# Kernel optimization log

Measured on AMD Instinct MI355X. Metric: run time of the kernel, lower is better.

Reference implementation:

```python
import jax, jax.numpy as jnp
import numpy as np

B, T, C, H = 4, 2048, 1024, 16
D = C // H  # head_dim = 64
ROPE_BASE = 10000.0


def _rope_cos_sin(T, D, dtype):
    # inv_freq: (D/2,), freqs: (T, D/2) -> cos/sin tiled to (T, D)
    inv_freq = 1.0 / (ROPE_BASE ** (jnp.arange(0, D, 2, dtype=jnp.float32) / D))
    freqs = jnp.arange(T, dtype=jnp.float32)[:, None] * inv_freq[None, :]
    emb = jnp.concatenate([freqs, freqs], axis=-1)  # (T, D)
    return jnp.cos(emb).astype(dtype), jnp.sin(emb).astype(dtype)


def _rotate_half(x):
    x1, x2 = jnp.split(x, 2, axis=-1)
    return jnp.concatenate([-x2, x1], axis=-1)


def setup_inputs() -> dict:
    key = jax.random.key(0)
    k1, k2, k3 = jax.random.split(key, 3)
    x = jax.random.normal(k1, (B, T, C), dtype=jnp.float32)
    W_qkv = jax.random.normal(k2, (C, 3 * C), dtype=jnp.float32) * (C ** -0.5)
    b_qkv = jnp.zeros((3 * C,), dtype=jnp.float32)
    W_out = jax.random.normal(k3, (C, C), dtype=jnp.float32) * (C ** -0.5)
    b_out = jnp.zeros((C,), dtype=jnp.float32)
    return {"x": x, "W_qkv": W_qkv, "b_qkv": b_qkv, "W_out": W_out, "b_out": b_out}


def reference(x, W_qkv, b_qkv, W_out, b_out):
    Bx, Tx, Cx = x.shape
    qkv = x @ W_qkv + b_qkv                                   # (B, T, 3C)
    qkv = qkv.reshape(Bx, Tx, 3, H, D).transpose(2, 0, 3, 1, 4)  # (3, B, H, T, D)
    q, k, v = qkv[0], qkv[1], qkv[2]

    cos, sin = _rope_cos_sin(Tx, D, x.dtype)                  # (T, D) each
    q = q * cos + _rotate_half(q) * sin
    k = k * cos + _rotate_half(k) * sin

    # NOTE: original code has no 1/sqrt(D) scaling — faithful reproduction.
    att = jnp.einsum('bhtd,bhsd->bhts', q, k)                 # (B, H, T, T)
    causal = jnp.tril(jnp.ones((Tx, Tx), dtype=bool))
    att = jnp.where(causal[None, None, :, :], att, -jnp.inf)
    att = jax.nn.softmax(att, axis=-1)
    y = jnp.einsum('bhts,bhsd->bhtd', att, v)                 # (B, H, T, D)
    y = y.transpose(0, 2, 1, 3).reshape(Bx, Tx, Cx)
    return y @ W_out + b_out
```

## Files before the change

kernel.cpp:

```cpp
#include <hip/hip_runtime.h>
#include <math.h>

#define NB    4
#define T_SEQ 2048
#define CDIM  1024
#define NH    16
#define DH    64
#define NQKV  3072

typedef short bf16x8 __attribute__((ext_vector_type(8)));
typedef float f32x4  __attribute__((ext_vector_type(4)));

#define GLOBAL_AS __attribute__((address_space(1)))
#define LDS_AS    __attribute__((address_space(3)))

__device__ __forceinline__ void async16(const void* g, void* l) {
  __builtin_amdgcn_global_load_lds((const GLOBAL_AS void*)g, (LDS_AS void*)l, 16, 0, 0);
}

__device__ __forceinline__ unsigned short f2bf(float f) {
  unsigned u = __float_as_uint(f);
  unsigned r = u + 0x7FFF + ((u >> 16) & 1);
  return (unsigned short)(r >> 16);
}

#define SWZ8(row, c) ((((row) << 3) | ((c) ^ ((row) & 7))) << 3)

#define BARRIER()  asm volatile("s_barrier" ::: "memory")
#define VMCNT(n)   asm volatile("s_waitcnt vmcnt(" #n ")" ::: "memory")

__device__ __forceinline__ void transpose_tile32(
    const float* __restrict__ in, unsigned short* __restrict__ out,
    int K, int N, int bx, int by, float (*tile)[33], int tid) {
  int n0 = bx << 5, k0 = by << 5;
  int r  = tid >> 3;
  int c4 = (tid & 7) << 2;
  float4 v = *(const float4*)&in[(size_t)(k0 + r) * N + n0 + c4];
  tile[r][c4 + 0] = v.x; tile[r][c4 + 1] = v.y;
  tile[r][c4 + 2] = v.z; tile[r][c4 + 3] = v.w;
  __syncthreads();
  ushort4 o;
  o.x = f2bf(tile[c4 + 0][r]); o.y = f2bf(tile[c4 + 1][r]);
  o.z = f2bf(tile[c4 + 2][r]); o.w = f2bf(tile[c4 + 3][r]);
  *(ushort4*)&out[(size_t)(n0 + r) * K + k0 + c4] = o;
}

__global__ __launch_bounds__(256) void prep_fused(
    const float* __restrict__ x, unsigned short* __restrict__ xb,
    const float* __restrict__ W_qkv, unsigned short* __restrict__ wqt,
    const float* __restrict__ W_out, unsigned short* __restrict__ wot,
    float2* __restrict__ rope) {
  __shared__ float tile[32][33];
  int blk = blockIdx.x;
  int tid = threadIdx.x;
  if (blk < 8192) {
    int i = blk * 256 + tid;
    float4 v = ((const float4*)x)[i];
    ushort4 o;
    o.x = f2bf(v.x); o.y = f2bf(v.y); o.z = f2bf(v.z); o.w = f2bf(v.w);
    ((ushort4*)xb)[i] = o;
  } else if (blk < 11264) {
    int local = blk - 8192;
    transpose_tile32(W_qkv, wqt, CDIM, NQKV, local % 96, local / 96, tile, tid);
  } else if (blk < 12288) {
    int local = blk - 11264;
    transpose_tile32(W_out, wot, CDIM, CDIM, local & 31, local >> 5, tile, tid);
  } else {
    int i = (blk - 12288) * 256 + tid;
    int t = i >> 5, d = i & 31;
    float inv = expf((float)d * -0.28782313662425572f);
    float s, c;
    sincosf((float)t * inv, &s, &c);
    rope[i] = make_float2(c, s);
  }
}

#define STAGE(kt, b)                                                          \
  { const unsigned short* sa_ = aSrc + (kt) * 64;                             \
    const unsigned short* sb_ = bSrc + (kt) * 64;                             \
    async16(sa_,          &As[b][d0]);                                        \
    async16(sa_ + 65536,  &As[b][d0 + 4096]);                                 \
    async16(sb_,          &Bs[b][d0]);                                        \
    async16(sb_ + 65536,  &Bs[b][d0 + 4096]);                                 \
    async16(sb_ + 131072, &Bs[b][d0 + 8192]);                                 \
    async16(sb_ + 196608, &Bs[b][d0 + 12288]); }

#define GEMM_PIPE(Aptr, Btptr)                                                \
  int tid = threadIdx.x;                                                      \
  int wave = tid >> 6, lane = tid & 63;                                       \
  int wm = wave >> 2, wn = wave & 3;                                          \
  int col = lane & 15, quad = lane >> 4;                                      \
  int srow = tid >> 3;                                                        \
  int schunk = (tid & 7) ^ (srow & 7);                                        \
  const unsigned short* aSrc = &Aptr[(size_t)(m0 + srow) * CDIM + schunk * 8];\
  const unsigned short* bSrc = &Btptr[(size_t)(n0 + srow) * CDIM + schunk * 8];\
  int d0 = wave * 512;      \
  f32x4 acc[4][4];                                                            \
  _Pragma("unroll") for (int mt = 0; mt < 4; ++mt)                            \
  _Pragma("unroll") for (int nt = 0; nt < 4; ++nt)                            \
    acc[mt][nt] = (f32x4){0.f, 0.f, 0.f, 0.f};                                \
  STAGE(0, 0)                                                                 \
  STAGE(1, 1)                                                                 \
  _Pragma("unroll")                                                           \
  for (int t = 0; t < 16; ++t) {                                              \
    if (t < 15) { VMCNT(6); } else { VMCNT(0); }                              \
    BARRIER();                                                                \
    if (t + 2 < 16) STAGE(t + 2, (t + 2) % 3)                                 \
    const short* A_ = As[t % 3];                                              \
    const short* B_ = Bs[t % 3];                                              \
    _Pragma("unroll") for (int ks = 0; ks < 2; ++ks) {                        \
      bf16x8 af[4], bfr[4];                                                   \
      _Pragma("unroll") for (int mt = 0; mt < 4; ++mt)                        \
        af[mt] = *(const bf16x8*)&A_[SWZ8(wm * 64 + mt * 16 + col,            \
                                          ks * 4 + quad)];                    \
      _Pragma("unroll") for (int nt = 0; nt < 4; ++nt)                        \
        bfr[nt] = *(const bf16x8*)&B_[SWZ8(wn * 64 + nt * 16 + col,           \
                                           ks * 4 + quad)];                   \
      __builtin_amdgcn_s_setprio(1);                                          \
      _Pragma("unroll") for (int mt = 0; mt < 4; ++mt)                        \
        _Pragma("unroll") for (int nt = 0; nt < 4; ++nt)                      \
          acc[mt][nt] = __builtin_amdgcn_mfma_f32_16x16x32_bf16(              \
              af[mt], bfr[nt], acc[mt][nt], 0, 0, 0);                         \
      __builtin_amdgcn_s_setprio(0);                                          \
    }                                                                         \
  }

__global__ __launch_bounds__(512, 2) void gemm_qkv_mfma(
    const unsigned short* __restrict__ A, const unsigned short* __restrict__ Bt,
    const float* __restrict__ bias, const float2* __restrict__ rope,
    unsigned short* __restrict__ qb, unsigned short* __restrict__ kb,
    unsigned short* __restrict__ vtb) {
  __shared__ short As[3][128 * 64];
  __shared__ short Bs[3][256 * 64];
  int orig = blockIdx.x;
  int wg = (orig & 7) * 96 + (orig >> 3);
  int m0 = (wg / 12) << 7, n0 = (wg % 12) << 8;
  GEMM_PIPE(A, Bt)
  int nn = n0 + wn * 64;
  int which = nn >> 10;
  int h = (nn >> 6) & 15;
  float bv[4];
#pragma unroll
  for (int nt = 0; nt < 4; ++nt) bv[nt] = bias[nn + nt * 16 + col];
  if (which < 2) {
    unsigned short* dst = (which == 0) ? qb : kb;
#pragma unroll
    for (int mt = 0; mt < 4; ++mt) {
#pragma unroll
      for (int r = 0; r < 4; ++r) {
        int m = m0 + wm * 64 + mt * 16 + quad * 4 + r;
        int bidx = m >> 11, t = m & 2047;
        float x0 = acc[mt][0][r] + bv[0];
        float x1 = acc[mt][1][r] + bv[1];
        float x2 = acc[mt][2][r] + bv[2];
        float x3 = acc[mt][3][r] + bv[3];
        float2 cs0 = rope[(t << 5) + col];
        float2 cs1 = rope[(t << 5) + col + 16];
        size_t ro = (((size_t)bidx * NH + h) * T_SEQ + t) * DH;
        dst[ro + col]      = f2bf(x0 * cs0.x - x2 * cs0.y);
        dst[ro + col + 16] = f2bf(x1 * cs1.x - x3 * cs1.y);
        dst[ro + col + 32] = f2bf(x2 * cs0.x + x0 * cs0.y);
        dst[ro + col + 48] = f2bf(x3 * cs1.x + x1 * cs1.y);
      }
    }
  } else {
    BARRIER();
    short* vt_tile = &Bs[0][0] + wave * (64 * 72);
#pragma unroll
    for (int nt = 0; nt < 4; ++nt) {
#pragma unroll
      for (int mt = 0; mt < 4; ++mt) {
        float y0 = acc[mt][nt][0] + bv[nt];
        float y1 = acc[mt][nt][1] + bv[nt];
        float y2 = acc[mt][nt][2] + bv[nt];
        float y3 = acc[mt][nt][3] + bv[nt];
        unsigned w0, w1;
        asm("v_cvt_pk_bf16_f32 %0, %1, %2" : "=v"(w0) : "v"(y0), "v"(y1));
        asm("v_cvt_pk_bf16_f32 %0, %1, %2" : "=v"(w1) : "v"(y2), "v"(y3));
        *(uint2*)&vt_tile[(nt * 16 + col) * 72 + mt * 16 + quad * 4] =
            make_uint2(w0, w1);
      }
    }
    int mbase = m0 + wm * 64;
    int bidx = mbase >> 11, t0v = mbase & 2047;
    size_t vbase = ((size_t)(bidx * NH + h) * DH) * T_SEQ;
#pragma unroll
    for (int u = 0; u < 8; ++u) {
      int f = u * 64 + lane;
      int d = f >> 3, c = f & 7;
      bf16x8 o = *(const bf16x8*)&vt_tile[d * 72 + c * 8];
      *(bf16x8*)&vtb[vbase + (size_t)d * T_SEQ + t0v + c * 8] = o;
    }
  }
}

__global__ __launch_bounds__(512, 2) void gemm_out_mfma(
    const unsigned short* __restrict__ A, const unsigned short* __restrict__ Bt,
    const float* __restrict__ bias, float* __restrict__ out) {
  __shared__ short As[3][128 * 64];
  __shared__ short Bs[3][256 * 64];
  int orig = blockIdx.x;
  int wg = (orig & 7) * 32 + (orig >> 3);
  int m0 = (wg >> 2) << 7, n0 = (wg & 3) << 8;
  GEMM_PIPE(A, Bt)
#pragma unroll
  for (int nt = 0; nt < 4; ++nt) {
    int n = n0 + wn * 64 + nt * 16 + col;
    float bv = bias[n];
#pragma unroll
    for (int mt = 0; mt < 4; ++mt) {
#pragma unroll
      for (int r = 0; r < 4; ++r) {
        int m = m0 + wm * 64 + mt * 16 + quad * 4 + r;
        out[(size_t)m * CDIM + n] = acc[mt][nt][r] + bv;
      }
    }
  }
}

__global__ __launch_bounds__(256) void attn_mfma(
    const unsigned short* __restrict__ qg, const unsigned short* __restrict__ kg,
    const unsigned short* __restrict__ vtg, unsigned short* __restrict__ yb) {
  __shared__ short Ks[2][64 * 64];
  __shared__ short Vts[2][64 * 64];
  __shared__ short Ps[4][32 * 64];
  int tid = threadIdx.x;
  int wave = tid >> 6, lane = tid & 63;
  int col = lane & 15, quad = lane >> 4;
  int bh = blockIdx.x;
  int qblk = 15 - (int)blockIdx.y;
  int qb0 = qblk << 7;
  size_t base = (size_t)bh * (T_SEQ * DH);

  bf16x8 qreg[2][2];
#pragma unroll
  for (int nt = 0; nt < 2; ++nt)
#pragma unroll
    for (int kc = 0; kc < 2; ++kc)
      qreg[nt][kc] = *(const bf16x8*)&qg[base +
          (size_t)(qb0 + wave * 32 + nt * 16 + col) * DH + kc * 32 + quad * 8];

  bf16x8 ones;
#pragma unroll
  for (int j = 0; j < 8; ++j) ones[j] = (short)0x3F80;

  f32x4 oc[2][4], lsum[2];
#pragma unroll
  for (int mq = 0; mq < 2; ++mq) {
    lsum[mq] = (f32x4){0.f, 0.f, 0.f, 0.f};
#pragma unroll
    for (int dt = 0; dt < 4; ++dt) oc[mq][dt] = (f32x4){0.f, 0.f, 0.f, 0.f};
  }

  int qlo = qb0 + wave * 32;
  int qhi = qlo + 31;
  int nrounds = qblk + 1;
  for (int rr = 0; rr < nrounds; ++rr) {
    __syncthreads();
#pragma unroll
    for (int v = 0; v < 2; ++v) {
      int s_ = (rr * 2 + v) << 6;
#pragma unroll
      for (int u = 0; u < 2; ++u) {
        int ff = u * 256 + wave * 64 + lane;
        int row = ff >> 3, cl = ff & 7;
        int cg = cl ^ (row & 7);
        async16(&kg[base + (size_t)(s_ + row) * DH + cg * 8],
                &Ks[v][(u * 256 + wave * 64) * 8]);
        async16(&vtg[base + (size_t)row * T_SEQ + s_ + cg * 8],
                &Vts[v][(u * 256 + wave * 64) * 8]);
      }
    }
    __syncthreads();

#pragma unroll
    for (int v = 0; v < 2; ++v) {
      int kb = rr * 2 + v;
      int s0 = kb << 6;
      if (s0 > qhi) continue;
      const short* K_ = Ks[v];
      const short* V_ = Vts[v];

      f32x4 sc[4][2];
#pragma unroll
      for (int mf = 0; mf < 4; ++mf)
#pragma unroll
        for (int nt = 0; nt < 2; ++nt) sc[mf][nt] = (f32x4){0.f, 0.f, 0.f, 0.f};
#pragma unroll
      for (int kc = 0; kc < 2; ++kc) {
#pragma unroll
        for (int mf = 0; mf < 4; ++mf) {
          bf16x8 ak = *(const bf16x8*)&K_[SWZ8(mf * 16 + col, kc * 4 + quad)];
          sc[mf][0] = __builtin_amdgcn_mfma_f32_16x16x32_bf16(ak, qreg[0][kc], sc[mf][0], 0, 0, 0);
          sc[mf][1] = __builtin_amdgcn_mfma_f32_16x16x32_bf16(ak, qreg[1][kc], sc[mf][1], 0, 0, 0);
        }
      }

      if (s0 + 63 > qlo) {
#pragma unroll
        for (int mf = 0; mf < 4; ++mf) {
          int kbase = s0 + mf * 16 + quad * 4;
#pragma unroll
          for (int nt = 0; nt < 2; ++nt) {
            int qq = qlo + nt * 16 + col;
#pragma unroll
            for (int r = 0; r < 4; ++r)
              if (kbase + r > qq) sc[mf][nt][r] = -3.0e38f;
          }
        }
      }

#pragma unroll
      for (int nt = 0; nt < 2; ++nt) {
        int row = nt * 16 + col;
        int rb = row << 6;
        int sw = row & 7;
#pragma unroll
        for (int mf = 0; mf < 4; ++mf) {
          float p0 = __expf(sc[mf][nt][0]);
          float p1 = __expf(sc[mf][nt][1]);
          float p2 = __expf(sc[mf][nt][2]);
          float p3 = __expf(sc[mf][nt][3]);
          unsigned w0, w1;
          asm("v_cvt_pk_bf16_f32 %0, %1, %2" : "=v"(w0) : "v"(p0), "v"(p1));
          asm("v_cvt_pk_bf16_f32 %0, %1, %2" : "=v"(w1) : "v"(p2), "v"(p3));
          int chunk = (mf << 1) | (quad >> 1);
          int off = rb + (((chunk ^ sw) << 3) | ((quad & 1) << 2));
          *(uint2*)&Ps[wave][off] = make_uint2(w0, w1);
        }
      }

#pragma unroll
      for (int kc = 0; kc < 2; ++kc) {
        bf16x8 ap0 = *(const bf16x8*)&Ps[wave][SWZ8(col,      kc * 4 + quad)];
        bf16x8 ap1 = *(const bf16x8*)&Ps[wave][SWZ8(16 + col, kc * 4 + quad)];
        lsum[0] = __builtin_amdgcn_mfma_f32_16x16x32_bf16(ap0, ones, lsum[0], 0, 0, 0);
        lsum[1] = __builtin_amdgcn_mfma_f32_16x16x32_bf16(ap1, ones, lsum[1], 0, 0, 0);
#pragma unroll
        for (int dt = 0; dt < 4; ++dt) {
          bf16x8 vb = *(const bf16x8*)&V_[SWZ8(dt * 16 + col, kc * 4 + quad)];
          oc[0][dt] = __builtin_amdgcn_mfma_f32_16x16x32_bf16(ap0, vb, oc[0][dt], 0, 0, 0);
          oc[1][dt] = __builtin_amdgcn_mfma_f32_16x16x32_bf16(ap1, vb, oc[1][dt], 0, 0, 0);
        }
      }
    }
  }

  int b = bh >> 4, h = bh & 15;
#pragma unroll
  for (int mq = 0; mq < 2; ++mq)
#pragma unroll
    for (int dt = 0; dt < 4; ++dt) {
      int d = dt * 16 + col;
#pragma unroll
      for (int r = 0; r < 4; ++r) {
        int t = qb0 + wave * 32 + mq * 16 + quad * 4 + r;
        yb[(((size_t)b * T_SEQ + t) * NH + h) * DH + d] =
            f2bf(oc[mq][dt][r] / lsum[mq][r]);
      }
    }
}

extern "C" void kernel_launch(void* const* d_in, const int* in_sizes, int n_in,
                              void* d_out, int out_size, void* d_ws, size_t ws_size,
                              hipStream_t stream) {
  const float* x     = (const float*)d_in[0];
  const float* W_qkv = (const float*)d_in[1];
  const float* b_qkv = (const float*)d_in[2];
  const float* W_out = (const float*)d_in[3];
  const float* b_out = (const float*)d_in[4];
  float* out = (float*)d_out;

  const size_t per = (size_t)NB * NH * T_SEQ * DH;
  unsigned short* xb  = (unsigned short*)d_ws;
  unsigned short* qb  = xb + per;
  unsigned short* kbf = qb + per;
  unsigned short* vbf = kbf + per;
  unsigned short* vtb = vbf + per;
  unsigned short* yb  = vtb + per;
  unsigned short* wqt = yb + per;
  unsigned short* wot = wqt + (size_t)NQKV * CDIM;
  float2* rope = (float2*)(wot + (size_t)CDIM * CDIM);

  prep_fused<<<12544, 256, 0, stream>>>(x, xb, W_qkv, wqt, W_out, wot, rope);
  gemm_qkv_mfma<<<768, 512, 0, stream>>>(xb, wqt, b_qkv, rope, qb, kbf, vtb);
  attn_mfma<<<dim3(NB * NH, T_SEQ / 128), 256, 0, stream>>>(qb, kbf, vtb, yb);
  gemm_out_mfma<<<256, 512, 0, stream>>>(yb, wot, b_out, out);
}
```

Before: 236.5 us.

## Load QKV GEMM B operand directly from global into registers, shrink LDS

In the QKV projection GEMM the weight (B) tile is no longer staged through LDS. Each wave now reads its bf16x8 B fragments straight from global memory inside the k-loop, and only the A tile stays in the triple-buffered async LDS pipeline. The V-transpose epilogue is reworked into two passes over a smaller per-wave scratch in the A buffer, and the launch-bounds occupancy hint is raised from 2 to 6 blocks. The aim is to cut LDS footprint and barrier-covered staging traffic so more blocks fit per CU. The cost is unprefetched global loads on the critical path, B reads duplicated across waves, and register pressure from the higher occupancy hint.

```diff
diff --git a/kernel.cpp b/kernel.cpp
--- a/kernel.cpp
+++ b/kernel.cpp
@@ -75,67 +75,67 @@
   }
 }
 
-#define STAGE(kt, b)                                                          \
-  { const unsigned short* sa_ = aSrc + (kt) * 64;                             \
-    const unsigned short* sb_ = bSrc + (kt) * 64;                             \
-    async16(sa_,          &As[b][d0]);                                        \
-    async16(sa_ + 65536,  &As[b][d0 + 4096]);                                 \
-    async16(sb_,          &Bs[b][d0]);                                        \
-    async16(sb_ + 65536,  &Bs[b][d0 + 4096]);                                 \
-    async16(sb_ + 131072, &Bs[b][d0 + 8192]);                                 \
-    async16(sb_ + 196608, &Bs[b][d0 + 12288]); }
-
-#define GEMM_PIPE(Aptr, Btptr)                                                \
-  int tid = threadIdx.x;                                                      \
-  int wave = tid >> 6, lane = tid & 63;                                       \
-  int wm = wave >> 2, wn = wave & 3;                                          \
-  int col = lane & 15, quad = lane >> 4;                                      \
-  int srow = tid >> 3;                                                        \
-  int schunk = (tid & 7) ^ (srow & 7);                                        \
-  const unsigned short* aSrc = &Aptr[(size_t)(m0 + srow) * CDIM + schunk * 8];\
-  const unsigned short* bSrc = &Btptr[(size_t)(n0 + srow) * CDIM + schunk * 8];\
-  int d0 = wave * 512;      \
-  f32x4 acc[4][4];                                                            \
-  _Pragma("unroll") for (int mt = 0; mt < 4; ++mt)                            \
-  _Pragma("unroll") for (int nt = 0; nt < 4; ++nt)                            \
-    acc[mt][nt] = (f32x4){0.f, 0.f, 0.f, 0.f};                                \
-  STAGE(0, 0)                                                                 \
-  STAGE(1, 1)                                                                 \
-  _Pragma("unroll")                                                           \
-  for (int t = 0; t < 16; ++t) {                                              \
-    if (t < 15) { VMCNT(6); } else { VMCNT(0); }                              \
-    BARRIER();                                                                \
-    if (t + 2 < 16) STAGE(t + 2, (t + 2) % 3)                                 \
-    const short* A_ = As[t % 3];                                              \
-    const short* B_ = Bs[t % 3];                                              \
-    _Pragma("unroll") for (int ks = 0; ks < 2; ++ks) {                        \
-      bf16x8 af[4], bfr[4];                                                   \
-      _Pragma("unroll") for (int mt = 0; mt < 4; ++mt)                        \
-        af[mt] = *(const bf16x8*)&A_[SWZ8(wm * 64 + mt * 16 + col,            \
-                                          ks * 4 + quad)];                    \
-      _Pragma("unroll") for (int nt = 0; nt < 4; ++nt)                        \
-        bfr[nt] = *(const bf16x8*)&B_[SWZ8(wn * 64 + nt * 16 + col,           \
-                                           ks * 4 + quad)];                   \
-      __builtin_amdgcn_s_setprio(1);                                          \
-      _Pragma("unroll") for (int mt = 0; mt < 4; ++mt)                        \
-        _Pragma("unroll") for (int nt = 0; nt < 4; ++nt)                      \
-          acc[mt][nt] = __builtin_amdgcn_mfma_f32_16x16x32_bf16(              \
-              af[mt], bfr[nt], acc[mt][nt], 0, 0, 0);                         \
-      __builtin_amdgcn_s_setprio(0);                                          \
-    }                                                                         \
-  }
-
-__global__ __launch_bounds__(512, 2) void gemm_qkv_mfma(
+__global__ __launch_bounds__(512, 6) void gemm_qkv_mfma(
     const unsigned short* __restrict__ A, const unsigned short* __restrict__ Bt,
     const float* __restrict__ bias, const float2* __restrict__ rope,
     unsigned short* __restrict__ qb, unsigned short* __restrict__ kb,
     unsigned short* __restrict__ vtb) {
   __shared__ short As[3][128 * 64];
-  __shared__ short Bs[3][256 * 64];
   int orig = blockIdx.x;
   int wg = (orig & 7) * 96 + (orig >> 3);
   int m0 = (wg / 12) << 7, n0 = (wg % 12) << 8;
-  GEMM_PIPE(A, Bt)
+  int tid = threadIdx.x;
+  int wave = tid >> 6, lane = tid & 63;
+  int wm = wave >> 2, wn = wave & 3;
+  int col = lane & 15, quad = lane >> 4;
+  int srow = tid >> 3;
+  int schunk = (tid & 7) ^ (srow & 7);
+  const unsigned short* aSrc = &A[(size_t)(m0 + srow) * CDIM + schunk * 8];
+  int d0 = wave * 512;
+  const unsigned short* bRow[4];
+#pragma unroll
+  for (int nt = 0; nt < 4; ++nt)
+    bRow[nt] = &Bt[(size_t)(n0 + wn * 64 + nt * 16 + col) * CDIM + quad * 8];
+
+  f32x4 acc[4][4];
+#pragma unroll
+  for (int mt = 0; mt < 4; ++mt)
+#pragma unroll
+    for (int nt = 0; nt < 4; ++nt) acc[mt][nt] = (f32x4){0.f, 0.f, 0.f, 0.f};
+
+#define STAGE_A(kt, b)                                                        \
+  { const unsigned short* sa_ = aSrc + (kt) * 64;                             \
+    async16(sa_,         &As[b][d0]);                                         \
+    async16(sa_ + 65536, &As[b][d0 + 4096]); }
+
+  STAGE_A(0, 0)
+  STAGE_A(1, 1)
+#pragma unroll
+  for (int t = 0; t < 16; ++t) {
+    if (t < 15) { VMCNT(2); } else { VMCNT(0); }
+    BARRIER();
+    if (t + 2 < 16) STAGE_A(t + 2, (t + 2) % 3)
+    const short* A_ = As[t % 3];
+#pragma unroll
+    for (int ks = 0; ks < 2; ++ks) {
+      bf16x8 af[4], bfr[4];
+#pragma unroll
+      for (int mt = 0; mt < 4; ++mt)
+        af[mt] = *(const bf16x8*)&A_[SWZ8(wm * 64 + mt * 16 + col, ks * 4 + quad)];
+#pragma unroll
+      for (int nt = 0; nt < 4; ++nt)
+        bfr[nt] = *(const bf16x8*)&bRow[nt][t * 64 + ks * 32];
+      __builtin_amdgcn_s_setprio(1);
+#pragma unroll
+      for (int mt = 0; mt < 4; ++mt)
+#pragma unroll
+        for (int nt = 0; nt < 4; ++nt)
+          acc[mt][nt] = __builtin_amdgcn_mfma_f32_16x16x32_bf16(
+              af[mt], bfr[nt], acc[mt][nt], 0, 0, 0);
+      __builtin_amdgcn_s_setprio(0);
+    }
+  }
+
   int nn = n0 + wn * 64;
   int which = nn >> 10;
   int h = (nn >> 6) & 15;
@@ -165,34 +165,48 @@
     }
   } else {
     BARRIER();
-    short* vt_tile = &Bs[0][0] + wave * (64 * 72);
-#pragma unroll
-    for (int nt = 0; nt < 4; ++nt) {
-#pragma unroll
-      for (int mt = 0; mt < 4; ++mt) {
-        float y0 = acc[mt][nt][0] + bv[nt];
-        float y1 = acc[mt][nt][1] + bv[nt];
-        float y2 = acc[mt][nt][2] + bv[nt];
-        float y3 = acc[mt][nt][3] + bv[nt];
-        unsigned w0, w1;
-        asm("v_cvt_pk_bf16_f32 %0, %1, %2" : "=v"(w0) : "v"(y0), "v"(y1));
-        asm("v_cvt_pk_bf16_f32 %0, %1, %2" : "=v"(w1) : "v"(y2), "v"(y3));
-        *(uint2*)&vt_tile[(nt * 16 + col) * 72 + mt * 16 + quad * 4] =
-            make_uint2(w0, w1);
-      }
-    }
+    short* scratch = (short*)As + wave * 2304;
     int mbase = m0 + wm * 64;
     int bidx = mbase >> 11, t0v = mbase & 2047;
     size_t vbase = ((size_t)(bidx * NH + h) * DH) * T_SEQ;
 #pragma unroll
-    for (int u = 0; u < 8; ++u) {
-      int f = u * 64 + lane;
-      int d = f >> 3, c = f & 7;
-      bf16x8 o = *(const bf16x8*)&vt_tile[d * 72 + c * 8];
-      *(bf16x8*)&vtb[vbase + (size_t)d * T_SEQ + t0v + c * 8] = o;
-    }
-  }
-}
+    for (int p = 0; p < 2; ++p) {
+#pragma unroll
+      for (int half = 0; half < 2; ++half) {
+        int nt = p * 2 + half;
+#pragma unroll
+        for (int mt = 0; mt < 4; ++mt) {
+          float y0 = acc[mt][nt][0] + bv[nt];
+          float y1 = acc[mt][nt][1] + bv[nt];
+          float y2 = acc[mt][nt][2] + bv[nt];
+          float y3 = acc[mt][nt][3] + bv[nt];
+          unsigned w0, w1;
+          asm("v_cvt_pk_bf16_f32 %0, %1, %2" : "=v"(w0) : "v"(y0), "v"(y1));
+          asm("v_cvt_pk_bf16_f32 %0, %1, %2" : "=v"(w1) : "v"(y2), "v"(y3));
+          *(uint2*)&scratch[(half * 16 + col) * 72 + mt * 16 + quad * 4] =
+              make_uint2(w0, w1);
+        }
+      }
+#pragma unroll
+      for (int u = 0; u < 4; ++u) {
+        int f = u * 64 + lane;
+        int dl = f >> 3, c = f & 7;
+        bf16x8 o = *(const bf16x8*)&scratch[dl * 72 + c * 8];
+        *(bf16x8*)&vtb[vbase + (size_t)(p * 32 + dl) * T_SEQ + t0v + c * 8] = o;
+      }
+    }
+  }
+}
+
+#define STAGE(kt, b)                                                          \
+  { const unsigned short* sa_ = aSrc + (kt) * 64;                             \
+    const unsigned short* sb_ = bSrc + (kt) * 64;                             \
+    async16(sa_,          &As[b][d0]);                                        \
+    async16(sa_ + 65536,  &As[b][d0 + 4096]);                                 \
+    async16(sb_,          &Bs[b][d0]);                                        \
+    async16(sb_ + 65536,  &Bs[b][d0 + 4096]);                                 \
+    async16(sb_ + 131072, &Bs[b][d0 + 8192]);                                 \
+    async16(sb_ + 196608, &Bs[b][d0 + 12288]); }
 
 __global__ __launch_bounds__(512, 2) void gemm_out_mfma(
     const unsigned short* __restrict__ A, const unsigned short* __restrict__ Bt,
@@ -202,7 +216,48 @@
   int orig = blockIdx.x;
   int wg = (orig & 7) * 32 + (orig >> 3);
   int m0 = (wg >> 2) << 7, n0 = (wg & 3) << 8;
-  GEMM_PIPE(A, Bt)
+  int tid = threadIdx.x;
+  int wave = tid >> 6, lane = tid & 63;
+  int wm = wave >> 2, wn = wave & 3;
+  int col = lane & 15, quad = lane >> 4;
+  int srow = tid >> 3;
+  int schunk = (tid & 7) ^ (srow & 7);
+  const unsigned short* aSrc = &A[(size_t)(m0 + srow) * CDIM + schunk * 8];
+  const unsigned short* bSrc = &Bt[(size_t)(n0 + srow) * CDIM + schunk * 8];
+  int d0 = wave * 512;
+  f32x4 acc[4][4];
+#pragma unroll
+  for (int mt = 0; mt < 4; ++mt)
+#pragma unroll
+    for (int nt = 0; nt < 4; ++nt) acc[mt][nt] = (f32x4){0.f, 0.f, 0.f, 0.f};
+  STAGE(0, 0)
+  STAGE(1, 1)
+#pragma unroll
+  for (int t = 0; t < 16; ++t) {
+    if (t < 15) { VMCNT(6); } else { VMCNT(0); }
+    BARRIER();
+    if (t + 2 < 16) STAGE(t + 2, (t + 2) % 3)
+    const short* A_ = As[t % 3];
+    const short* B_ = Bs[t % 3];
+#pragma unroll
+    for (int ks = 0; ks < 2; ++ks) {
+      bf16x8 af[4], bfr[4];
+#pragma unroll
+      for (int mt = 0; mt < 4; ++mt)
+        af[mt] = *(const bf16x8*)&A_[SWZ8(wm * 64 + mt * 16 + col, ks * 4 + quad)];
+#pragma unroll
+      for (int nt = 0; nt < 4; ++nt)
+        bfr[nt] = *(const bf16x8*)&B_[SWZ8(wn * 64 + nt * 16 + col, ks * 4 + quad)];
+      __builtin_amdgcn_s_setprio(1);
+#pragma unroll
+      for (int mt = 0; mt < 4; ++mt)
+#pragma unroll
+        for (int nt = 0; nt < 4; ++nt)
+          acc[mt][nt] = __builtin_amdgcn_mfma_f32_16x16x32_bf16(
+              af[mt], bfr[nt], acc[mt][nt], 0, 0, 0);
+      __builtin_amdgcn_s_setprio(0);
+    }
+  }
 #pragma unroll
   for (int nt = 0; nt < 4; ++nt) {
     int n = n0 + wn * 64 + nt * 16 + col;
```

Result: slower. 726.8 us (+207.2%).
